# Performance work log

Hardware: AMD Instinct MI355X
Metric: run time of the kernel (lower is better)

The kernel has to match this reference:

```python
import jax, jax.numpy as jnp
import numpy as np

N = 100000   # nodes
E = 3200000  # edges
G = 64       # graphs in batch
F_IN = 128   # num_features
H = 8        # hidden per TAGConv (hard-coded in module)
K = 3        # TAGConv hops (PyG default)
L = 3        # num_layers


def setup_inputs() -> dict:
    key = jax.random.key(0)
    ks = jax.random.split(key, 8)
    x = jax.random.normal(ks[0], (N, F_IN), dtype=jnp.float32)
    edge_index = jax.random.randint(ks[1], (2, E), 0, N, dtype=jnp.int32)
    batch = jnp.sort(jax.random.randint(ks[2], (N,), 0, G, dtype=jnp.int32))
    edge_weight = jax.random.uniform(ks[3], (E,), dtype=jnp.float32)
    W1 = jax.random.normal(ks[4], ((K + 1) * F_IN, H), dtype=jnp.float32) * 0.05
    W2 = jax.random.normal(ks[5], ((K + 1) * H, H), dtype=jnp.float32) * 0.1
    W3 = jax.random.normal(ks[6], ((K + 1) * H, H), dtype=jnp.float32) * 0.1
    fcW = jax.random.normal(ks[7], (2 * L * H, 2), dtype=jnp.float32) * 0.1
    return {
        'x': x, 'edge_index': edge_index, 'batch': batch,
        'edge_weight': edge_weight,
        'W1': W1, 'b1': jnp.zeros((H,), jnp.float32),
        'W2': W2, 'b2': jnp.zeros((H,), jnp.float32),
        'W3': W3, 'b3': jnp.zeros((H,), jnp.float32),
        'fcW': fcW, 'fcb': jnp.zeros((2,), jnp.float32),
    }


def _tag_conv(h, src, dst, norm, W, b):
    # TAGConv: concat [h, T h, T^2 h, T^3 h] then one linear (== sum of per-hop linears)
    xs = [h]
    for _ in range(K):
        h = jax.ops.segment_sum(h[src] * norm[:, None], dst, num_segments=N)
        xs.append(h)
    return jnp.concatenate(xs, axis=-1) @ W + b


def reference(x, edge_index, batch, edge_weight, W1, b1, W2, b2, W3, b3, fcW, fcb):
    src, dst = edge_index[0], edge_index[1]
    # GCN symmetric normalization, no self loops (PyG TAGConv default)
    deg = jax.ops.segment_sum(edge_weight, dst, num_segments=N)
    safe = jnp.where(deg > 0, deg, 1.0)
    dis = jnp.where(deg > 0, jax.lax.rsqrt(safe), 0.0)
    norm = dis[src] * edge_weight * dis[dst]  # [E]

    h = jax.nn.relu(_tag_conv(x, src, dst, norm, W1, b1))
    xs = [h]
    for (W, b) in ((W2, b2), (W3, b3)):
        h = jax.nn.relu(_tag_conv(h, src, dst, norm, W, b))
        xs.append(h)
    jk = jnp.concatenate(xs, axis=-1)  # [N, L*H] = [N, 24]

    # global max pool + global mean pool per graph
    gmax = jax.ops.segment_max(jk, batch, num_segments=G)
    gmax = jnp.where(jnp.isfinite(gmax), gmax, 0.0)
    gsum = jax.ops.segment_sum(jk, batch, num_segments=G)
    cnt = jax.ops.segment_sum(jnp.ones((N,), jk.dtype), batch, num_segments=G)
    gmean = gsum / jnp.maximum(cnt, 1.0)[:, None]
    pooled = jnp.concatenate([gmax, gmean], axis=-1)  # [G, 48]
    return pooled @ fcW + fcb  # [G, 2]
```

## Files before the change

### kernel.cpp

```cpp
#include <hip/hip_runtime.h>

static inline int div_up(int a, int b){ return (a + b - 1) / b; }

constexpr int FIN = 128;
constexpr unsigned long long DEG_MASK = ((unsigned long long)1 << 48) - 1;


__global__ __launch_bounds__(256) void count_gemm1_k(
    const int* __restrict__ dst, const float* __restrict__ w,
    unsigned long long* __restrict__ packed, unsigned short* __restrict__ ie, int E, int Eb,
    const float* __restrict__ x, const float* __restrict__ W,
    float* __restrict__ z0, float* __restrict__ z1,
    float* __restrict__ z2, float* __restrict__ z3, int n)
{
    if (blockIdx.x < (unsigned)Eb){
        int e = blockIdx.x * 256 + threadIdx.x;
        if (e >= E) return;
        int d = dst[e];
        unsigned long long add = ((unsigned long long)1 << 48)
                               | (unsigned long long)(w[e] * 4294967296.0f);
        unsigned long long old = atomicAdd(&packed[d], add);
        ie[e] = (unsigned short)(old >> 48);
    } else {
        int node = (blockIdx.x - Eb) * 256 + threadIdx.x;
        if (node >= n) return;
        const float4* xr = (const float4*)(x + (size_t)node * FIN);
        float acc[32];
        #pragma unroll
        for (int o = 0; o < 32; ++o) acc[o] = 0.f;
        #pragma unroll 2
        for (int fc = 0; fc < FIN / 4; ++fc){
            float4 xv = xr[fc];
            #pragma unroll
            for (int jj = 0; jj < 4; ++jj){
                float xs = jj == 0 ? xv.x : jj == 1 ? xv.y : jj == 2 ? xv.z : xv.w;
                int f = fc * 4 + jj;
                #pragma unroll
                for (int k = 0; k < 4; ++k)
                    #pragma unroll
                    for (int h = 0; h < 8; ++h)
                        acc[k * 8 + h] = fmaf(xs, W[((size_t)(k * FIN + f)) * 8 + h], acc[k * 8 + h]);
            }
        }
        float* zp[4] = {z0, z1, z2, z3};
        #pragma unroll
        for (int k = 0; k < 4; ++k){
            float4* zr = (float4*)(zp[k] + (size_t)node * 8);
            zr[0] = make_float4(acc[k*8+0], acc[k*8+1], acc[k*8+2], acc[k*8+3]);
            zr[1] = make_float4(acc[k*8+4], acc[k*8+5], acc[k*8+6], acc[k*8+7]);
        }
    }
}

__global__ __launch_bounds__(256) void scan_sum_k(const unsigned long long* __restrict__ packed,
    int* __restrict__ bsum, int n)
{
    __shared__ int lds[256];
    int t = threadIdx.x;
    int base = blockIdx.x * 1024 + t * 4;
    int s = 0;
    #pragma unroll
    for (int i = 0; i < 4; ++i) if (base + i < n) s += (int)(packed[base + i] >> 48);
    lds[t] = s; __syncthreads();
    for (int o = 128; o > 0; o >>= 1){
        if (t < o) lds[t] += lds[t + o];
        __syncthreads();
    }
    if (t == 0) bsum[blockIdx.x] = lds[0];
}

__global__ __launch_bounds__(256) void scan_block_k(int* __restrict__ bsum, int nb,
    int* __restrict__ rowptr, int n, int Etot)
{
    __shared__ int lds[256];
    int t = threadIdx.x;
    int v = (t < nb) ? bsum[t] : 0;
    lds[t] = v; __syncthreads();
    for (int o = 1; o < 256; o <<= 1){
        int add = (t >= o) ? lds[t - o] : 0;
        __syncthreads();
        lds[t] += add;
        __syncthreads();
    }
    if (t < nb) bsum[t] = lds[t] - v;
    if (t == 0) rowptr[n] = Etot;
}

__global__ __launch_bounds__(256) void scan_apply_k(const unsigned long long* __restrict__ packed,
    const int* __restrict__ bsum, int* __restrict__ rowptr, float* __restrict__ dis, int n)
{
    __shared__ int lds[256];
    int t = threadIdx.x;
    int base = blockIdx.x * 1024 + t * 4;
    int v[4]; int ts = 0;
    unsigned long long pk[4];
    #pragma unroll
    for (int i = 0; i < 4; ++i){
        pk[i] = (base + i < n) ? packed[base + i] : 0ull;
        v[i] = (int)(pk[i] >> 48); ts += v[i];
    }
    lds[t] = ts; __syncthreads();
    for (int o = 1; o < 256; o <<= 1){
        int add = (t >= o) ? lds[t - o] : 0;
        __syncthreads();
        lds[t] += add;
        __syncthreads();
    }
    int pre = lds[t] - ts + bsum[blockIdx.x];
    #pragma unroll
    for (int i = 0; i < 4; ++i){
        if (base + i < n){
            rowptr[base + i] = pre;
            float d = (float)(pk[i] & DEG_MASK) * (1.0f / 4294967296.0f);
            dis[base + i] = d > 0.f ? rsqrtf(d) : 0.f;
        }
        pre += v[i];
    }
}

__global__ __launch_bounds__(256) void scatter_k(const int* __restrict__ src,
    const int* __restrict__ dst, const float* __restrict__ w,
    const float* __restrict__ dis, const int* __restrict__ rowptr,
    const unsigned short* __restrict__ ie, int2* __restrict__ edges, int E)
{
    int e = blockIdx.x * 256 + threadIdx.x;
    if (e >= E) return;
    int s = src[e], d = dst[e];
    float nm = dis[s] * w[e] * dis[d];
    int pos = rowptr[d] + (int)ie[e];
    edges[pos] = make_int2(s, __float_as_int(nm));
}


__global__ __launch_bounds__(256) void gemm_small_k(const float* __restrict__ hin,
    const float* __restrict__ W, float* __restrict__ z0, float* __restrict__ z1,
    float* __restrict__ z2, float* __restrict__ z3, int n)
{
    int node = blockIdx.x * 256 + threadIdx.x;
    if (node >= n) return;
    const float4* hr = (const float4*)(hin + (size_t)node * 8);
    float4 p0 = hr[0], p1 = hr[1];
    float hv[8] = {p0.x, p0.y, p0.z, p0.w, p1.x, p1.y, p1.z, p1.w};
    float acc[32];
    #pragma unroll
    for (int o = 0; o < 32; ++o) acc[o] = 0.f;
    #pragma unroll
    for (int f = 0; f < 8; ++f)
        #pragma unroll
        for (int k = 0; k < 4; ++k)
            #pragma unroll
            for (int h = 0; h < 8; ++h)
                acc[k * 8 + h] = fmaf(hv[f], W[(k * 8 + f) * 8 + h], acc[k * 8 + h]);
    float* zp[4] = {z0, z1, z2, z3};
    #pragma unroll
    for (int k = 0; k < 4; ++k){
        float4* zr = (float4*)(zp[k] + (size_t)node * 8);
        zr[0] = make_float4(acc[k*8+0], acc[k*8+1], acc[k*8+2], acc[k*8+3]);
        zr[1] = make_float4(acc[k*8+4], acc[k*8+5], acc[k*8+6], acc[k*8+7]);
    }
}


template<bool RELU, bool GEMM>
__global__ __launch_bounds__(256) void prop_k(const int2* __restrict__ edges,
    const int* __restrict__ rowptr, const float* __restrict__ uin,
    const float* __restrict__ addv, const float* __restrict__ bias,
    float* __restrict__ uout, const float* __restrict__ Wn,
    float* __restrict__ zo0, float* __restrict__ zo1,
    float* __restrict__ zo2, float* __restrict__ zo3, int n)
{
    int t = blockIdx.x * 256 + threadIdx.x;
    int node = t >> 3, g = t & 7;
    if (node >= n) return;
    int r0 = rowptr[node], r1 = rowptr[node + 1];
    float acc = 0.f;
    int j = r0;
    for (; j + 4 <= r1; j += 4){
        int2 e0 = edges[j], e1 = edges[j+1], e2 = edges[j+2], e3 = edges[j+3];
        float a0 = uin[(size_t)e0.x * 8 + g];
        float a1 = uin[(size_t)e1.x * 8 + g];
        float a2 = uin[(size_t)e2.x * 8 + g];
        float a3 = uin[(size_t)e3.x * 8 + g];
        acc = fmaf(__int_as_float(e0.y), a0, acc);
        acc = fmaf(__int_as_float(e1.y), a1, acc);
        acc = fmaf(__int_as_float(e2.y), a2, acc);
        acc = fmaf(__int_as_float(e3.y), a3, acc);
    }
    for (; j < r1; ++j){
        int2 e0 = edges[j];
        acc = fmaf(__int_as_float(e0.y), uin[(size_t)e0.x * 8 + g], acc);
    }
    float v = addv[(size_t)node * 8 + g] + acc;
    if (RELU) v = fmaxf(v + bias[g], 0.f);
    uout[(size_t)node * 8 + g] = v;
    if (GEMM){
        int lane = threadIdx.x & 63;
        int gbase = lane & ~7;
        float hrow[8];
        #pragma unroll
        for (int f = 0; f < 8; ++f) hrow[f] = __shfl(v, gbase + f);
        int k = g >> 1;
        float zv[4];
        #pragma unroll
        for (int q = 0; q < 4; ++q){
            int h = (g & 1) * 4 + q;
            float s = 0.f;
            #pragma unroll
            for (int f = 0; f < 8; ++f)
                s = fmaf(hrow[f], Wn[(k * 8 + f) * 8 + h], s);
            zv[q] = s;
        }
        float* zp = (k == 0) ? zo0 : (k == 1) ? zo1 : (k == 2) ? zo2 : zo3;
        *(float4*)(zp + (size_t)node * 8 + (g & 1) * 4) = make_float4(zv[0], zv[1], zv[2], zv[3]);
    }
}


__global__ __launch_bounds__(256) void pool_k(const float* __restrict__ h1,
    const float* __restrict__ h2, const float* __restrict__ h3,
    const int* __restrict__ batch, unsigned* __restrict__ gmaxb,
    float* __restrict__ gsum, int* __restrict__ gcnt, int n)
{
    int t = blockIdx.x * 256 + threadIdx.x;
    int lane = threadIdx.x & 63;
    bool valid = (t < n);
    int b = valid ? batch[t] : -1;
    float v[24];
    #pragma unroll
    for (int q = 0; q < 24; ++q) v[q] = 0.f;
    if (valid){
        const float4* p1 = (const float4*)(h1 + (size_t)t * 8);
        const float4* p2 = (const float4*)(h2 + (size_t)t * 8);
        const float4* p3 = (const float4*)(h3 + (size_t)t * 8);
        float4 a0 = p1[0], a1 = p1[1], c0 = p2[0], c1 = p2[1], d0 = p3[0], d1 = p3[1];
        v[0]=a0.x; v[1]=a0.y; v[2]=a0.z; v[3]=a0.w; v[4]=a1.x; v[5]=a1.y; v[6]=a1.z; v[7]=a1.w;
        v[8]=c0.x; v[9]=c0.y; v[10]=c0.z; v[11]=c0.w; v[12]=c1.x; v[13]=c1.y; v[14]=c1.z; v[15]=c1.w;
        v[16]=d0.x; v[17]=d0.y; v[18]=d0.z; v[19]=d0.w; v[20]=d1.x; v[21]=d1.y; v[22]=d1.z; v[23]=d1.w;
    }
    int bl0 = __shfl(b, 0);
    bool uni = __all(b == bl0);
    if (uni){
        if (bl0 >= 0){
            #pragma unroll
            for (int q = 0; q < 24; ++q){
                float s = v[q], m = v[q];
                #pragma unroll
                for (int o = 1; o < 64; o <<= 1){
                    s += __shfl_xor(s, o);
                    m = fmaxf(m, __shfl_xor(m, o));
                }
                if (lane == 0){
                    atomicAdd(&gsum[bl0 * 24 + q], s);
                    atomicMax(&gmaxb[bl0 * 24 + q], __float_as_uint(m));
                }
            }
            if (lane == 0) atomicAdd(&gcnt[bl0], 64);
        }
    } else if (valid){
        #pragma unroll
        for (int q = 0; q < 24; ++q){
            atomicAdd(&gsum[b * 24 + q], v[q]);
            atomicMax(&gmaxb[b * 24 + q], __float_as_uint(v[q]));
        }
        atomicAdd(&gcnt[b], 1);
    }
}

__global__ __launch_bounds__(64) void fc_k(const unsigned* __restrict__ gmaxb,
    const float* __restrict__ gsum, const int* __restrict__ gcnt,
    const float* __restrict__ fcW, const float* __restrict__ fcb,
    float* __restrict__ out, int G)
{
    int g = threadIdx.x;
    if (g >= G) return;
    float pooled[48];
    #pragma unroll
    for (int q = 0; q < 24; ++q) pooled[q] = __uint_as_float(gmaxb[g * 24 + q]);
    float c = (float)gcnt[g];
    if (c < 1.f) c = 1.f;
    float inv = 1.f / c;
    #pragma unroll
    for (int q = 0; q < 24; ++q) pooled[24 + q] = gsum[g * 24 + q] * inv;
    float o0 = fcb[0], o1 = fcb[1];
    #pragma unroll
    for (int j = 0; j < 48; ++j){
        o0 = fmaf(pooled[j], fcW[j * 2 + 0], o0);
        o1 = fmaf(pooled[j], fcW[j * 2 + 1], o1);
    }
    out[g * 2 + 0] = o0;
    out[g * 2 + 1] = o1;
}


extern "C" void kernel_launch(void* const* d_in, const int* in_sizes, int n_in,
                              void* d_out, int out_size, void* d_ws, size_t ws_size,
                              hipStream_t stream)
{
    const float* x    = (const float*)d_in[0];
    const int*   ei   = (const int*)d_in[1];
    const int*   batch= (const int*)d_in[2];
    const float* w    = (const float*)d_in[3];
    const float* W1   = (const float*)d_in[4];
    const float* b1   = (const float*)d_in[5];
    const float* W2   = (const float*)d_in[6];
    const float* b2   = (const float*)d_in[7];
    const float* W3   = (const float*)d_in[8];
    const float* b3   = (const float*)d_in[9];
    const float* fcW  = (const float*)d_in[10];
    const float* fcb  = (const float*)d_in[11];
    float* out = (float*)d_out;

    const int N = in_sizes[2];
    const int E = in_sizes[3];
    const int G = out_size / 2;
    const int* src = ei;
    const int* dst = ei + E;

    char* base = (char*)d_ws;
    size_t off = 0;
    auto alloc = [&](size_t bytes) -> char* {
        char* r = base + off;
        off += (bytes + 255) & ~(size_t)255;
        return r;
    };
    unsigned long long* packed = (unsigned long long*)alloc((size_t)N * 8);
    unsigned* gmaxb  = (unsigned*)alloc((size_t)G * 24 * 4);
    float*    gsum   = (float*)   alloc((size_t)G * 24 * 4);
    int*      gcnt   = (int*)     alloc((size_t)G * 4);
    size_t zero_bytes = off;
    float*    dis    = (float*)   alloc((size_t)N * 4);
    unsigned short* ie = (unsigned short*)alloc((size_t)E * 2);
    int*      rowptr = (int*)     alloc((size_t)(N + 1) * 4);
    int*      bsum   = (int*)     alloc(256 * 4);
    int2*     edges  = (int2*)    alloc((size_t)E * 8);
    float*    zA[4], *zB[4];
    for (int k = 0; k < 4; ++k) zA[k] = (float*)alloc((size_t)N * 8 * 4);
    float*    u0     = (float*)   alloc((size_t)N * 8 * 4);
    float*    u1     = (float*)   alloc((size_t)N * 8 * 4);
    float*    h1     = (float*)   alloc((size_t)N * 8 * 4);
    float*    h2     = (float*)   alloc((size_t)N * 8 * 4);
    float*    h3     = (float*)   alloc((size_t)N * 8 * 4);
    for (int k = 0; k < 4; ++k) zB[k] = (float*)alloc((size_t)N * 8 * 4);
    bool fused = (off <= ws_size);
    if (!fused) for (int k = 0; k < 4; ++k) zB[k] = zA[k];

    hipMemsetAsync(d_ws, 0, zero_bytes, stream);

    dim3 blk(256);
    int Eb = div_up(E, 256), Nb = div_up(N, 256);
    count_gemm1_k<<<Eb + Nb, blk, 0, stream>>>(dst, w, packed, ie, E, Eb,
                                               x, W1, zA[0], zA[1], zA[2], zA[3], N);
    int nb = div_up(N, 1024);
    scan_sum_k  <<<nb, blk, 0, stream>>>(packed, bsum, N);
    scan_block_k<<<1,  blk, 0, stream>>>(bsum, nb, rowptr, N, E);
    scan_apply_k<<<nb, blk, 0, stream>>>(packed, bsum, rowptr, dis, N);
    scatter_k<<<div_up(E, 256), blk, 0, stream>>>(src, dst, w, dis, rowptr, ie, edges, E);

    int pb = div_up(N * 8, 256);
    prop_k<false,false><<<pb, blk, 0, stream>>>(edges, rowptr, zA[3], zA[2], nullptr, u0, nullptr, nullptr, nullptr, nullptr, nullptr, N);
    prop_k<false,false><<<pb, blk, 0, stream>>>(edges, rowptr, u0, zA[1], nullptr, u1, nullptr, nullptr, nullptr, nullptr, nullptr, N);
    if (fused){
        prop_k<true,true ><<<pb, blk, 0, stream>>>(edges, rowptr, u1, zA[0], b1, h1, W2, zB[0], zB[1], zB[2], zB[3], N);
    } else {
        prop_k<true,false><<<pb, blk, 0, stream>>>(edges, rowptr, u1, zA[0], b1, h1, nullptr, nullptr, nullptr, nullptr, nullptr, N);
        gemm_small_k<<<div_up(N, 256), blk, 0, stream>>>(h1, W2, zB[0], zB[1], zB[2], zB[3], N);
    }
    prop_k<false,false><<<pb, blk, 0, stream>>>(edges, rowptr, zB[3], zB[2], nullptr, u0, nullptr, nullptr, nullptr, nullptr, nullptr, N);
    prop_k<false,false><<<pb, blk, 0, stream>>>(edges, rowptr, u0, zB[1], nullptr, u1, nullptr, nullptr, nullptr, nullptr, nullptr, N);
    if (fused){
        prop_k<true,true ><<<pb, blk, 0, stream>>>(edges, rowptr, u1, zB[0], b2, h2, W3, zA[0], zA[1], zA[2], zA[3], N);
    } else {
        prop_k<true,false><<<pb, blk, 0, stream>>>(edges, rowptr, u1, zB[0], b2, h2, nullptr, nullptr, nullptr, nullptr, nullptr, N);
        gemm_small_k<<<div_up(N, 256), blk, 0, stream>>>(h2, W3, zA[0], zA[1], zA[2], zA[3], N);
    }
    prop_k<false,false><<<pb, blk, 0, stream>>>(edges, rowptr, zA[3], zA[2], nullptr, u0, nullptr, nullptr, nullptr, nullptr, nullptr, N);
    prop_k<false,false><<<pb, blk, 0, stream>>>(edges, rowptr, u0, zA[1], nullptr, u1, nullptr, nullptr, nullptr, nullptr, nullptr, N);
    prop_k<true,false><<<pb, blk, 0, stream>>>(edges, rowptr, u1, zA[0], b3, h3, nullptr, nullptr, nullptr, nullptr, nullptr, N);

    pool_k<<<div_up(N, 256), blk, 0, stream>>>(h1, h2, h3, batch, gmaxb, gsum, gcnt, N);
    fc_k<<<1, 64, 0, stream>>>(gmaxb, gsum, gcnt, fcW, fcb, out, G);
}
```

Baseline: 772.1 us.

## Assign one wavefront per node in propagation and split count/gemm1 kernels

Result: slower. 953.8 us (+23.5%).

```diff
diff --git a/kernel.cpp b/kernel.cpp
--- a/kernel.cpp
+++ b/kernel.cpp
@@ -6,50 +6,17 @@
 constexpr unsigned long long DEG_MASK = ((unsigned long long)1 << 48) - 1;
 
 
-__global__ __launch_bounds__(256) void count_gemm1_k(
-    const int* __restrict__ dst, const float* __restrict__ w,
-    unsigned long long* __restrict__ packed, unsigned short* __restrict__ ie, int E, int Eb,
-    const float* __restrict__ x, const float* __restrict__ W,
-    float* __restrict__ z0, float* __restrict__ z1,
-    float* __restrict__ z2, float* __restrict__ z3, int n)
-{
-    if (blockIdx.x < (unsigned)Eb){
-        int e = blockIdx.x * 256 + threadIdx.x;
-        if (e >= E) return;
-        int d = dst[e];
-        unsigned long long add = ((unsigned long long)1 << 48)
-                               | (unsigned long long)(w[e] * 4294967296.0f);
-        unsigned long long old = atomicAdd(&packed[d], add);
-        ie[e] = (unsigned short)(old >> 48);
-    } else {
-        int node = (blockIdx.x - Eb) * 256 + threadIdx.x;
-        if (node >= n) return;
-        const float4* xr = (const float4*)(x + (size_t)node * FIN);
-        float acc[32];
-        #pragma unroll
-        for (int o = 0; o < 32; ++o) acc[o] = 0.f;
-        #pragma unroll 2
-        for (int fc = 0; fc < FIN / 4; ++fc){
-            float4 xv = xr[fc];
-            #pragma unroll
-            for (int jj = 0; jj < 4; ++jj){
-                float xs = jj == 0 ? xv.x : jj == 1 ? xv.y : jj == 2 ? xv.z : xv.w;
-                int f = fc * 4 + jj;
-                #pragma unroll
-                for (int k = 0; k < 4; ++k)
-                    #pragma unroll
-                    for (int h = 0; h < 8; ++h)
-                        acc[k * 8 + h] = fmaf(xs, W[((size_t)(k * FIN + f)) * 8 + h], acc[k * 8 + h]);
-            }
-        }
-        float* zp[4] = {z0, z1, z2, z3};
-        #pragma unroll
-        for (int k = 0; k < 4; ++k){
-            float4* zr = (float4*)(zp[k] + (size_t)node * 8);
-            zr[0] = make_float4(acc[k*8+0], acc[k*8+1], acc[k*8+2], acc[k*8+3]);
-            zr[1] = make_float4(acc[k*8+4], acc[k*8+5], acc[k*8+6], acc[k*8+7]);
-        }
-    }
+__global__ __launch_bounds__(256) void count_deg_k(const int* __restrict__ dst,
+    const float* __restrict__ w, unsigned long long* __restrict__ packed,
+    unsigned short* __restrict__ ie, int E)
+{
+    int e = blockIdx.x * 256 + threadIdx.x;
+    if (e >= E) return;
+    int d = dst[e];
+    unsigned long long add = ((unsigned long long)1 << 48)
+                           | (unsigned long long)(w[e] * 4294967296.0f);
+    unsigned long long old = atomicAdd(&packed[d], add);
+    ie[e] = (unsigned short)(old >> 48);
 }
 
 __global__ __launch_bounds__(256) void scan_sum_k(const unsigned long long* __restrict__ packed,
@@ -129,6 +96,40 @@
     float nm = dis[s] * w[e] * dis[d];
     int pos = rowptr[d] + (int)ie[e];
     edges[pos] = make_int2(s, __float_as_int(nm));
+}
+
+
+__global__ __launch_bounds__(256) void gemm1_k(const float* __restrict__ x,
+    const float* __restrict__ W, float* __restrict__ z0, float* __restrict__ z1,
+    float* __restrict__ z2, float* __restrict__ z3, int n)
+{
+    int node = blockIdx.x * 256 + threadIdx.x;
+    if (node >= n) return;
+    const float4* xr = (const float4*)(x + (size_t)node * FIN);
+    float acc[32];
+    #pragma unroll
+    for (int o = 0; o < 32; ++o) acc[o] = 0.f;
+    #pragma unroll 2
+    for (int fc = 0; fc < FIN / 4; ++fc){
+        float4 xv = xr[fc];
+        #pragma unroll
+        for (int jj = 0; jj < 4; ++jj){
+            float xs = jj == 0 ? xv.x : jj == 1 ? xv.y : jj == 2 ? xv.z : xv.w;
+            int f = fc * 4 + jj;
+            #pragma unroll
+            for (int k = 0; k < 4; ++k)
+                #pragma unroll
+                for (int h = 0; h < 8; ++h)
+                    acc[k * 8 + h] = fmaf(xs, W[((size_t)(k * FIN + f)) * 8 + h], acc[k * 8 + h]);
+        }
+    }
+    float* zp[4] = {z0, z1, z2, z3};
+    #pragma unroll
+    for (int k = 0; k < 4; ++k){
+        float4* zr = (float4*)(zp[k] + (size_t)node * 8);
+        zr[0] = make_float4(acc[k*8+0], acc[k*8+1], acc[k*8+2], acc[k*8+3]);
+        zr[1] = make_float4(acc[k*8+4], acc[k*8+5], acc[k*8+6], acc[k*8+7]);
+    }
 }
 
 
@@ -169,49 +170,35 @@
     float* __restrict__ zo0, float* __restrict__ zo1,
     float* __restrict__ zo2, float* __restrict__ zo3, int n)
 {
-    int t = blockIdx.x * 256 + threadIdx.x;
-    int node = t >> 3, g = t & 7;
+    int node = blockIdx.x * 4 + (threadIdx.x >> 6);
     if (node >= n) return;
+    int lane = threadIdx.x & 63;
+    int el = lane >> 3, g = lane & 7;
     int r0 = rowptr[node], r1 = rowptr[node + 1];
     float acc = 0.f;
-    int j = r0;
-    for (; j + 4 <= r1; j += 4){
-        int2 e0 = edges[j], e1 = edges[j+1], e2 = edges[j+2], e3 = edges[j+3];
-        float a0 = uin[(size_t)e0.x * 8 + g];
-        float a1 = uin[(size_t)e1.x * 8 + g];
-        float a2 = uin[(size_t)e2.x * 8 + g];
-        float a3 = uin[(size_t)e3.x * 8 + g];
-        acc = fmaf(__int_as_float(e0.y), a0, acc);
-        acc = fmaf(__int_as_float(e1.y), a1, acc);
-        acc = fmaf(__int_as_float(e2.y), a2, acc);
-        acc = fmaf(__int_as_float(e3.y), a3, acc);
-    }
-    for (; j < r1; ++j){
-        int2 e0 = edges[j];
-        acc = fmaf(__int_as_float(e0.y), uin[(size_t)e0.x * 8 + g], acc);
-    }
+    for (int j = r0 + el; j < r1; j += 8){
+        int2 rec = edges[j];
+        acc = fmaf(__int_as_float(rec.y), uin[(size_t)rec.x * 8 + g], acc);
+    }
+    acc += __shfl_xor(acc, 8);
+    acc += __shfl_xor(acc, 16);
+    acc += __shfl_xor(acc, 32);
     float v = addv[(size_t)node * 8 + g] + acc;
     if (RELU) v = fmaxf(v + bias[g], 0.f);
-    uout[(size_t)node * 8 + g] = v;
+    if (lane < 8) uout[(size_t)node * 8 + g] = v;
     if (GEMM){
-        int lane = threadIdx.x & 63;
-        int gbase = lane & ~7;
         float hrow[8];
         #pragma unroll
-        for (int f = 0; f < 8; ++f) hrow[f] = __shfl(v, gbase + f);
-        int k = g >> 1;
-        float zv[4];
-        #pragma unroll
-        for (int q = 0; q < 4; ++q){
-            int h = (g & 1) * 4 + q;
+        for (int f = 0; f < 8; ++f) hrow[f] = __shfl(v, f);
+        if (lane < 32){
+            int k = lane >> 3, h = lane & 7;
             float s = 0.f;
             #pragma unroll
             for (int f = 0; f < 8; ++f)
                 s = fmaf(hrow[f], Wn[(k * 8 + f) * 8 + h], s);
-            zv[q] = s;
-        }
-        float* zp = (k == 0) ? zo0 : (k == 1) ? zo1 : (k == 2) ? zo2 : zo3;
-        *(float4*)(zp + (size_t)node * 8 + (g & 1) * 4) = make_float4(zv[0], zv[1], zv[2], zv[3]);
+            float* zp = (k == 0) ? zo0 : (k == 1) ? zo1 : (k == 2) ? zo2 : zo3;
+            zp[(size_t)node * 8 + h] = s;
+        }
     }
 }
 
@@ -347,16 +334,15 @@
     hipMemsetAsync(d_ws, 0, zero_bytes, stream);
 
     dim3 blk(256);
-    int Eb = div_up(E, 256), Nb = div_up(N, 256);
-    count_gemm1_k<<<Eb + Nb, blk, 0, stream>>>(dst, w, packed, ie, E, Eb,
-                                               x, W1, zA[0], zA[1], zA[2], zA[3], N);
+    count_deg_k<<<div_up(E, 256), blk, 0, stream>>>(dst, w, packed, ie, E);
+    gemm1_k<<<div_up(N, 256), blk, 0, stream>>>(x, W1, zA[0], zA[1], zA[2], zA[3], N);
     int nb = div_up(N, 1024);
     scan_sum_k  <<<nb, blk, 0, stream>>>(packed, bsum, N);
     scan_block_k<<<1,  blk, 0, stream>>>(bsum, nb, rowptr, N, E);
     scan_apply_k<<<nb, blk, 0, stream>>>(packed, bsum, rowptr, dis, N);
     scatter_k<<<div_up(E, 256), blk, 0, stream>>>(src, dst, w, dis, rowptr, ie, edges, E);
 
-    int pb = div_up(N * 8, 256);
+    int pb = div_up(N, 4);
     prop_k<false,false><<<pb, blk, 0, stream>>>(edges, rowptr, zA[3], zA[2], nullptr, u0, nullptr, nullptr, nullptr, nullptr, nullptr, N);
     prop_k<false,false><<<pb, blk, 0, stream>>>(edges, rowptr, u0, zA[1], nullptr, u1, nullptr, nullptr, nullptr, nullptr, nullptr, N);
     if (fused){
```

## Privatize degree-count atomics into eight copies and unroll edge gather by eight

Applied to the files above, without the earlier changes.

Result: no change. 786.1 us (+1.8%).

```diff
diff --git a/kernel.cpp b/kernel.cpp
--- a/kernel.cpp
+++ b/kernel.cpp
@@ -6,53 +6,21 @@
 constexpr unsigned long long DEG_MASK = ((unsigned long long)1 << 48) - 1;
 
 
-__global__ __launch_bounds__(256) void count_gemm1_k(
-    const int* __restrict__ dst, const float* __restrict__ w,
-    unsigned long long* __restrict__ packed, unsigned short* __restrict__ ie, int E, int Eb,
-    const float* __restrict__ x, const float* __restrict__ W,
-    float* __restrict__ z0, float* __restrict__ z1,
-    float* __restrict__ z2, float* __restrict__ z3, int n)
-{
-    if (blockIdx.x < (unsigned)Eb){
-        int e = blockIdx.x * 256 + threadIdx.x;
-        if (e >= E) return;
-        int d = dst[e];
-        unsigned long long add = ((unsigned long long)1 << 48)
-                               | (unsigned long long)(w[e] * 4294967296.0f);
-        unsigned long long old = atomicAdd(&packed[d], add);
-        ie[e] = (unsigned short)(old >> 48);
-    } else {
-        int node = (blockIdx.x - Eb) * 256 + threadIdx.x;
-        if (node >= n) return;
-        const float4* xr = (const float4*)(x + (size_t)node * FIN);
-        float acc[32];
-        #pragma unroll
-        for (int o = 0; o < 32; ++o) acc[o] = 0.f;
-        #pragma unroll 2
-        for (int fc = 0; fc < FIN / 4; ++fc){
-            float4 xv = xr[fc];
-            #pragma unroll
-            for (int jj = 0; jj < 4; ++jj){
-                float xs = jj == 0 ? xv.x : jj == 1 ? xv.y : jj == 2 ? xv.z : xv.w;
-                int f = fc * 4 + jj;
-                #pragma unroll
-                for (int k = 0; k < 4; ++k)
-                    #pragma unroll
-                    for (int h = 0; h < 8; ++h)
-                        acc[k * 8 + h] = fmaf(xs, W[((size_t)(k * FIN + f)) * 8 + h], acc[k * 8 + h]);
-            }
-        }
-        float* zp[4] = {z0, z1, z2, z3};
-        #pragma unroll
-        for (int k = 0; k < 4; ++k){
-            float4* zr = (float4*)(zp[k] + (size_t)node * 8);
-            zr[0] = make_float4(acc[k*8+0], acc[k*8+1], acc[k*8+2], acc[k*8+3]);
-            zr[1] = make_float4(acc[k*8+4], acc[k*8+5], acc[k*8+6], acc[k*8+7]);
-        }
-    }
-}
-
-__global__ __launch_bounds__(256) void scan_sum_k(const unsigned long long* __restrict__ packed,
+__global__ __launch_bounds__(256) void count_deg_k(const int* __restrict__ dst,
+    const float* __restrict__ w, unsigned long long* __restrict__ packed8,
+    unsigned short* __restrict__ ie, int E, int N)
+{
+    int e = blockIdx.x * 256 + threadIdx.x;
+    if (e >= E) return;
+    int copy = blockIdx.x & 7;
+    int d = dst[e];
+    unsigned long long add = ((unsigned long long)1 << 48)
+                           | (unsigned long long)(w[e] * 4294967296.0f);
+    unsigned long long old = atomicAdd(&packed8[(size_t)copy * N + d], add);
+    ie[e] = (unsigned short)(old >> 48);
+}
+
+__global__ __launch_bounds__(256) void scan_sum_k(const unsigned long long* __restrict__ packed8,
     int* __restrict__ bsum, int n)
 {
     __shared__ int lds[256];
@@ -60,7 +28,13 @@
     int base = blockIdx.x * 1024 + t * 4;
     int s = 0;
     #pragma unroll
-    for (int i = 0; i < 4; ++i) if (base + i < n) s += (int)(packed[base + i] >> 48);
+    for (int i = 0; i < 4; ++i){
+        if (base + i < n){
+            #pragma unroll
+            for (int c = 0; c < 8; ++c)
+                s += (int)(packed8[(size_t)c * n + base + i] >> 48);
+        }
+    }
     lds[t] = s; __syncthreads();
     for (int o = 128; o > 0; o >>= 1){
         if (t < o) lds[t] += lds[t + o];
@@ -86,18 +60,28 @@
     if (t == 0) rowptr[n] = Etot;
 }
 
-__global__ __launch_bounds__(256) void scan_apply_k(const unsigned long long* __restrict__ packed,
-    const int* __restrict__ bsum, int* __restrict__ rowptr, float* __restrict__ dis, int n)
+__global__ __launch_bounds__(256) void scan_apply_k(const unsigned long long* __restrict__ packed8,
+    const int* __restrict__ bsum, int* __restrict__ rowptr, float* __restrict__ dis,
+    unsigned short* __restrict__ off16, int n)
 {
     __shared__ int lds[256];
     int t = threadIdx.x;
     int base = blockIdx.x * 1024 + t * 4;
     int v[4]; int ts = 0;
-    unsigned long long pk[4];
+    unsigned long long fx[4];
     #pragma unroll
     for (int i = 0; i < 4; ++i){
-        pk[i] = (base + i < n) ? packed[base + i] : 0ull;
-        v[i] = (int)(pk[i] >> 48); ts += v[i];
+        int cnt = 0; unsigned long long f = 0;
+        if (base + i < n){
+            #pragma unroll
+            for (int c = 0; c < 8; ++c){
+                unsigned long long p = packed8[(size_t)c * n + base + i];
+                off16[(size_t)c * n + base + i] = (unsigned short)cnt;
+                cnt += (int)(p >> 48);
+                f += (p & DEG_MASK);
+            }
+        }
+        v[i] = cnt; ts += cnt; fx[i] = f;
     }
     lds[t] = ts; __syncthreads();
     for (int o = 1; o < 256; o <<= 1){
@@ -111,7 +95,7 @@
     for (int i = 0; i < 4; ++i){
         if (base + i < n){
             rowptr[base + i] = pre;
-            float d = (float)(pk[i] & DEG_MASK) * (1.0f / 4294967296.0f);
+            float d = (float)fx[i] * (1.0f / 4294967296.0f);
             dis[base + i] = d > 0.f ? rsqrtf(d) : 0.f;
         }
         pre += v[i];
@@ -121,14 +105,50 @@
 __global__ __launch_bounds__(256) void scatter_k(const int* __restrict__ src,
     const int* __restrict__ dst, const float* __restrict__ w,
     const float* __restrict__ dis, const int* __restrict__ rowptr,
-    const unsigned short* __restrict__ ie, int2* __restrict__ edges, int E)
+    const unsigned short* __restrict__ ie, const unsigned short* __restrict__ off16,
+    int2* __restrict__ edges, int E, int N)
 {
     int e = blockIdx.x * 256 + threadIdx.x;
     if (e >= E) return;
+    int copy = blockIdx.x & 7;
     int s = src[e], d = dst[e];
     float nm = dis[s] * w[e] * dis[d];
-    int pos = rowptr[d] + (int)ie[e];
+    int pos = rowptr[d] + (int)off16[(size_t)copy * N + d] + (int)ie[e];
     edges[pos] = make_int2(s, __float_as_int(nm));
+}
+
+
+__global__ __launch_bounds__(256) void gemm1_k(const float* __restrict__ x,
+    const float* __restrict__ W, float* __restrict__ z0, float* __restrict__ z1,
+    float* __restrict__ z2, float* __restrict__ z3, int n)
+{
+    int node = blockIdx.x * 256 + threadIdx.x;
+    if (node >= n) return;
+    const float4* xr = (const float4*)(x + (size_t)node * FIN);
+    float acc[32];
+    #pragma unroll
+    for (int o = 0; o < 32; ++o) acc[o] = 0.f;
+    #pragma unroll 2
+    for (int fc = 0; fc < FIN / 4; ++fc){
+        float4 xv = xr[fc];
+        #pragma unroll
+        for (int jj = 0; jj < 4; ++jj){
+            float xs = jj == 0 ? xv.x : jj == 1 ? xv.y : jj == 2 ? xv.z : xv.w;
+            int f = fc * 4 + jj;
+            #pragma unroll
+            for (int k = 0; k < 4; ++k)
+                #pragma unroll
+                for (int h = 0; h < 8; ++h)
+                    acc[k * 8 + h] = fmaf(xs, W[((size_t)(k * FIN + f)) * 8 + h], acc[k * 8 + h]);
+        }
+    }
+    float* zp[4] = {z0, z1, z2, z3};
+    #pragma unroll
+    for (int k = 0; k < 4; ++k){
+        float4* zr = (float4*)(zp[k] + (size_t)node * 8);
+        zr[0] = make_float4(acc[k*8+0], acc[k*8+1], acc[k*8+2], acc[k*8+3]);
+        zr[1] = make_float4(acc[k*8+4], acc[k*8+5], acc[k*8+6], acc[k*8+7]);
+    }
 }
 
 
@@ -175,16 +195,25 @@
     int r0 = rowptr[node], r1 = rowptr[node + 1];
     float acc = 0.f;
     int j = r0;
-    for (; j + 4 <= r1; j += 4){
-        int2 e0 = edges[j], e1 = edges[j+1], e2 = edges[j+2], e3 = edges[j+3];
+    for (; j + 8 <= r1; j += 8){
+        int2 e0 = edges[j],   e1 = edges[j+1], e2 = edges[j+2], e3 = edges[j+3];
+        int2 e4 = edges[j+4], e5 = edges[j+5], e6 = edges[j+6], e7 = edges[j+7];
         float a0 = uin[(size_t)e0.x * 8 + g];
         float a1 = uin[(size_t)e1.x * 8 + g];
         float a2 = uin[(size_t)e2.x * 8 + g];
         float a3 = uin[(size_t)e3.x * 8 + g];
+        float a4 = uin[(size_t)e4.x * 8 + g];
+        float a5 = uin[(size_t)e5.x * 8 + g];
+        float a6 = uin[(size_t)e6.x * 8 + g];
+        float a7 = uin[(size_t)e7.x * 8 + g];
         acc = fmaf(__int_as_float(e0.y), a0, acc);
         acc = fmaf(__int_as_float(e1.y), a1, acc);
         acc = fmaf(__int_as_float(e2.y), a2, acc);
         acc = fmaf(__int_as_float(e3.y), a3, acc);
+        acc = fmaf(__int_as_float(e4.y), a4, acc);
+        acc = fmaf(__int_as_float(e5.y), a5, acc);
+        acc = fmaf(__int_as_float(e6.y), a6, acc);
+        acc = fmaf(__int_as_float(e7.y), a7, acc);
     }
     for (; j < r1; ++j){
         int2 e0 = edges[j];
@@ -323,13 +352,14 @@
         off += (bytes + 255) & ~(size_t)255;
         return r;
     };
-    unsigned long long* packed = (unsigned long long*)alloc((size_t)N * 8);
+    unsigned long long* packed8 = (unsigned long long*)alloc((size_t)N * 8 * 8);
     unsigned* gmaxb  = (unsigned*)alloc((size_t)G * 24 * 4);
     float*    gsum   = (float*)   alloc((size_t)G * 24 * 4);
     int*      gcnt   = (int*)     alloc((size_t)G * 4);
     size_t zero_bytes = off;
     float*    dis    = (float*)   alloc((size_t)N * 4);
-    unsigned short* ie = (unsigned short*)alloc((size_t)E * 2);
+    unsigned short* ie    = (unsigned short*)alloc((size_t)E * 2);
+    unsigned short* off16 = (unsigned short*)alloc((size_t)N * 8 * 2);
     int*      rowptr = (int*)     alloc((size_t)(N + 1) * 4);
     int*      bsum   = (int*)     alloc(256 * 4);
     int2*     edges  = (int2*)    alloc((size_t)E * 8);
@@ -347,14 +377,13 @@
     hipMemsetAsync(d_ws, 0, zero_bytes, stream);
 
     dim3 blk(256);
-    int Eb = div_up(E, 256), Nb = div_up(N, 256);
-    count_gemm1_k<<<Eb + Nb, blk, 0, stream>>>(dst, w, packed, ie, E, Eb,
-                                               x, W1, zA[0], zA[1], zA[2], zA[3], N);
+    count_deg_k<<<div_up(E, 256), blk, 0, stream>>>(dst, w, packed8, ie, E, N);
+    gemm1_k<<<div_up(N, 256), blk, 0, stream>>>(x, W1, zA[0], zA[1], zA[2], zA[3], N);
     int nb = div_up(N, 1024);
-    scan_sum_k  <<<nb, blk, 0, stream>>>(packed, bsum, N);
+    scan_sum_k  <<<nb, blk, 0, stream>>>(packed8, bsum, N);
     scan_block_k<<<1,  blk, 0, stream>>>(bsum, nb, rowptr, N, E);
-    scan_apply_k<<<nb, blk, 0, stream>>>(packed, bsum, rowptr, dis, N);
-    scatter_k<<<div_up(E, 256), blk, 0, stream>>>(src, dst, w, dis, rowptr, ie, edges, E);
+    scan_apply_k<<<nb, blk, 0, stream>>>(packed8, bsum, rowptr, dis, off16, N);
+    scatter_k<<<div_up(E, 256), blk, 0, stream>>>(src, dst, w, dis, rowptr, ie, off16, edges, E, N);
 
     int pb = div_up(N * 8, 256);
     prop_k<false,false><<<pb, blk, 0, stream>>>(edges, rowptr, zA[3], zA[2], nullptr, u0, nullptr, nullptr, nullptr, nullptr, nullptr, N);
```

## Split degree counting into edge-chunk launches, separate gemm1, unroll prop gather by 8

Applied to the files above, without the earlier changes.

New measurement: 792.6 us. +2.6%, slower.

```diff
diff --git a/kernel.cpp b/kernel.cpp
--- a/kernel.cpp
+++ b/kernel.cpp
@@ -6,50 +6,17 @@
 constexpr unsigned long long DEG_MASK = ((unsigned long long)1 << 48) - 1;
 
 
-__global__ __launch_bounds__(256) void count_gemm1_k(
-    const int* __restrict__ dst, const float* __restrict__ w,
-    unsigned long long* __restrict__ packed, unsigned short* __restrict__ ie, int E, int Eb,
-    const float* __restrict__ x, const float* __restrict__ W,
-    float* __restrict__ z0, float* __restrict__ z1,
-    float* __restrict__ z2, float* __restrict__ z3, int n)
-{
-    if (blockIdx.x < (unsigned)Eb){
-        int e = blockIdx.x * 256 + threadIdx.x;
-        if (e >= E) return;
-        int d = dst[e];
-        unsigned long long add = ((unsigned long long)1 << 48)
-                               | (unsigned long long)(w[e] * 4294967296.0f);
-        unsigned long long old = atomicAdd(&packed[d], add);
-        ie[e] = (unsigned short)(old >> 48);
-    } else {
-        int node = (blockIdx.x - Eb) * 256 + threadIdx.x;
-        if (node >= n) return;
-        const float4* xr = (const float4*)(x + (size_t)node * FIN);
-        float acc[32];
-        #pragma unroll
-        for (int o = 0; o < 32; ++o) acc[o] = 0.f;
-        #pragma unroll 2
-        for (int fc = 0; fc < FIN / 4; ++fc){
-            float4 xv = xr[fc];
-            #pragma unroll
-            for (int jj = 0; jj < 4; ++jj){
-                float xs = jj == 0 ? xv.x : jj == 1 ? xv.y : jj == 2 ? xv.z : xv.w;
-                int f = fc * 4 + jj;
-                #pragma unroll
-                for (int k = 0; k < 4; ++k)
-                    #pragma unroll
-                    for (int h = 0; h < 8; ++h)
-                        acc[k * 8 + h] = fmaf(xs, W[((size_t)(k * FIN + f)) * 8 + h], acc[k * 8 + h]);
-            }
-        }
-        float* zp[4] = {z0, z1, z2, z3};
-        #pragma unroll
-        for (int k = 0; k < 4; ++k){
-            float4* zr = (float4*)(zp[k] + (size_t)node * 8);
-            zr[0] = make_float4(acc[k*8+0], acc[k*8+1], acc[k*8+2], acc[k*8+3]);
-            zr[1] = make_float4(acc[k*8+4], acc[k*8+5], acc[k*8+6], acc[k*8+7]);
-        }
-    }
+__global__ __launch_bounds__(256) void count_deg_k(const int* __restrict__ dst,
+    const float* __restrict__ w, unsigned long long* __restrict__ packed,
+    unsigned short* __restrict__ ie, int e0, int e1)
+{
+    int e = e0 + blockIdx.x * 256 + threadIdx.x;
+    if (e >= e1) return;
+    int d = dst[e];
+    unsigned long long add = ((unsigned long long)1 << 48)
+                           | (unsigned long long)(w[e] * 4294967296.0f);
+    unsigned long long old = atomicAdd(&packed[d], add);
+    ie[e] = (unsigned short)(old >> 48);
 }
 
 __global__ __launch_bounds__(256) void scan_sum_k(const unsigned long long* __restrict__ packed,
@@ -129,6 +96,40 @@
     float nm = dis[s] * w[e] * dis[d];
     int pos = rowptr[d] + (int)ie[e];
     edges[pos] = make_int2(s, __float_as_int(nm));
+}
+
+
+__global__ __launch_bounds__(256) void gemm1_k(const float* __restrict__ x,
+    const float* __restrict__ W, float* __restrict__ z0, float* __restrict__ z1,
+    float* __restrict__ z2, float* __restrict__ z3, int n)
+{
+    int node = blockIdx.x * 256 + threadIdx.x;
+    if (node >= n) return;
+    const float4* xr = (const float4*)(x + (size_t)node * FIN);
+    float acc[32];
+    #pragma unroll
+    for (int o = 0; o < 32; ++o) acc[o] = 0.f;
+    #pragma unroll 2
+    for (int fc = 0; fc < FIN / 4; ++fc){
+        float4 xv = xr[fc];
+        #pragma unroll
+        for (int jj = 0; jj < 4; ++jj){
+            float xs = jj == 0 ? xv.x : jj == 1 ? xv.y : jj == 2 ? xv.z : xv.w;
+            int f = fc * 4 + jj;
+            #pragma unroll
+            for (int k = 0; k < 4; ++k)
+                #pragma unroll
+                for (int h = 0; h < 8; ++h)
+                    acc[k * 8 + h] = fmaf(xs, W[((size_t)(k * FIN + f)) * 8 + h], acc[k * 8 + h]);
+        }
+    }
+    float* zp[4] = {z0, z1, z2, z3};
+    #pragma unroll
+    for (int k = 0; k < 4; ++k){
+        float4* zr = (float4*)(zp[k] + (size_t)node * 8);
+        zr[0] = make_float4(acc[k*8+0], acc[k*8+1], acc[k*8+2], acc[k*8+3]);
+        zr[1] = make_float4(acc[k*8+4], acc[k*8+5], acc[k*8+6], acc[k*8+7]);
+    }
 }
 
 
@@ -175,16 +176,25 @@
     int r0 = rowptr[node], r1 = rowptr[node + 1];
     float acc = 0.f;
     int j = r0;
-    for (; j + 4 <= r1; j += 4){
-        int2 e0 = edges[j], e1 = edges[j+1], e2 = edges[j+2], e3 = edges[j+3];
+    for (; j + 8 <= r1; j += 8){
+        int2 e0 = edges[j],   e1 = edges[j+1], e2 = edges[j+2], e3 = edges[j+3];
+        int2 e4 = edges[j+4], e5 = edges[j+5], e6 = edges[j+6], e7 = edges[j+7];
         float a0 = uin[(size_t)e0.x * 8 + g];
         float a1 = uin[(size_t)e1.x * 8 + g];
         float a2 = uin[(size_t)e2.x * 8 + g];
         float a3 = uin[(size_t)e3.x * 8 + g];
+        float a4 = uin[(size_t)e4.x * 8 + g];
+        float a5 = uin[(size_t)e5.x * 8 + g];
+        float a6 = uin[(size_t)e6.x * 8 + g];
+        float a7 = uin[(size_t)e7.x * 8 + g];
         acc = fmaf(__int_as_float(e0.y), a0, acc);
         acc = fmaf(__int_as_float(e1.y), a1, acc);
         acc = fmaf(__int_as_float(e2.y), a2, acc);
         acc = fmaf(__int_as_float(e3.y), a3, acc);
+        acc = fmaf(__int_as_float(e4.y), a4, acc);
+        acc = fmaf(__int_as_float(e5.y), a5, acc);
+        acc = fmaf(__int_as_float(e6.y), a6, acc);
+        acc = fmaf(__int_as_float(e7.y), a7, acc);
     }
     for (; j < r1; ++j){
         int2 e0 = edges[j];
@@ -347,9 +357,13 @@
     hipMemsetAsync(d_ws, 0, zero_bytes, stream);
 
     dim3 blk(256);
-    int Eb = div_up(E, 256), Nb = div_up(N, 256);
-    count_gemm1_k<<<Eb + Nb, blk, 0, stream>>>(dst, w, packed, ie, E, Eb,
-                                               x, W1, zA[0], zA[1], zA[2], zA[3], N);
+    int Q = div_up(E, 4 * 256) * 256;
+    for (int p = 0; p < 4; ++p){
+        int e0 = p * Q, e1 = min(E, (p + 1) * Q);
+        if (e0 >= e1) break;
+        count_deg_k<<<div_up(e1 - e0, 256), blk, 0, stream>>>(dst, w, packed, ie, e0, e1);
+    }
+    gemm1_k<<<div_up(N, 256), blk, 0, stream>>>(x, W1, zA[0], zA[1], zA[2], zA[3], N);
     int nb = div_up(N, 1024);
     scan_sum_k  <<<nb, blk, 0, stream>>>(packed, bsum, N);
     scan_block_k<<<1,  blk, 0, stream>>>(bsum, nb, rowptr, N, E);
```
